# Performance work log

Measured on AMD Instinct MI355X. Metric: run time of the kernel, lower is better.

## Reference

```python
import jax, jax.numpy as jnp
import numpy as np

DIM = 512
HIDDEN = 512
HEADS = 8
HEAD_DIM = HIDDEN // HEADS
SCALE = HEAD_DIM ** -0.5
B, H, W = 2, 64, 64


def setup_inputs() -> dict:
    key = jax.random.key(0)
    ks = jax.random.split(key, 12)
    init = lambda k, shp: jax.random.normal(k, shp, dtype=jnp.float32) * 0.02
    return {
        "x": jax.random.normal(ks[0], (B, DIM, H, W), dtype=jnp.float32),
        "context": jax.random.normal(ks[1], (B, DIM, H, W), dtype=jnp.float32),
        # weights stored [in, out] so y = x @ W + b
        "Wi": init(ks[2], (DIM, HIDDEN)), "bi": jnp.zeros((HIDDEN,), jnp.float32),
        "Wc": init(ks[3], (DIM, HIDDEN)), "bc": jnp.zeros((HIDDEN,), jnp.float32),
        "Wq": init(ks[4], (HIDDEN, HIDDEN)),
        "Wk": init(ks[5], (HIDDEN, HIDDEN)),
        "Wv": init(ks[6], (HIDDEN, HIDDEN)),
        "Wo1": init(ks[7], (HIDDEN, HIDDEN)), "bo1": jnp.zeros((HIDDEN,), jnp.float32),
        "Wo2": init(ks[8], (HIDDEN, DIM)), "bo2": jnp.zeros((DIM,), jnp.float32),
    }


def reference(x, context, Wi, bi, Wc, bc, Wq, Wk, Wv, Wo1, bo1, Wo2, bo2):
    b, c, h, w = x.shape
    s = h * w
    x_seq = x.reshape(b, c, s).transpose(0, 2, 1)        # [B,S,C]
    ctx_seq = context.reshape(b, c, s).transpose(0, 2, 1)

    x_proj = x_seq @ Wi + bi                              # [B,S,Hid]
    ctx_proj = ctx_seq @ Wc + bc

    q = (x_proj @ Wq).reshape(b, s, HEADS, HEAD_DIM)      # [B,S,h,d]
    k = (ctx_proj @ Wk).reshape(b, s, HEADS, HEAD_DIM)
    v = (ctx_proj @ Wv).reshape(b, s, HEADS, HEAD_DIM)

    attn = jnp.einsum('bqhd,bkhd->bhqk', q, k) * SCALE    # [B,h,S,S]
    attn = jax.nn.softmax(attn, axis=-1)
    out = jnp.einsum('bhqk,bkhd->bqhd', attn, v).reshape(b, s, HIDDEN)

    out = jax.nn.gelu(out @ Wo1 + bo1, approximate=False) @ Wo2 + bo2  # [B,S,C]
    return out.transpose(0, 2, 1).reshape(b, c, h, w)
```

## Files before the change

### kernel.cpp

```cpp
#include <hip/hip_runtime.h>

#define SEQ 4096
#define CDIM 512
#define HID 512
#define NB 2
#define NHEADS 8

typedef float f32x4 __attribute__((ext_vector_type(4)));
typedef short bf16x8 __attribute__((ext_vector_type(8)));

static __device__ __forceinline__ short f2bf(float f) {
  unsigned u = __float_as_uint(f);
  u = (u + 0x7fffu + ((u >> 16) & 1u)) >> 16;
  return (short)u;
}
static __device__ __forceinline__ float bf2f(short h) {
  return __uint_as_float(((unsigned)(unsigned short)h) << 16);
}
static __device__ __forceinline__ unsigned pk2bf(float a, float b) {
  unsigned r;
  asm("v_cvt_pk_bf16_f32 %0, %1, %2" : "=v"(r) : "v"(a), "v"(b));
  return r;
}
typedef const __attribute__((address_space(1))) char gas_char;
typedef __attribute__((address_space(3))) char las_char;
static __device__ __forceinline__ void gll16(const char* g, char* l) {
  __builtin_amdgcn_global_load_lds((gas_char*)g, (las_char*)l, 16, 0, 0);
}

__global__ __launch_bounds__(256) void prep_w(
    const float* Wi, const float* Wc, const float* Wq, const float* Wk,
    const float* Wv, const float* Wo1, const float* Wo2,
    unsigned short* wth, unsigned short* wtl) {
  __shared__ float tile[32][33];
  const int z = blockIdx.z;
  const float* src;
  float scale = 1.0f;
  switch (z) {
    case 0: src = Wi; break;
    case 1: src = Wc; break;
    case 2: src = Wq; scale = 0.18033688011112042f; break;
    case 3: src = Wk; break;
    case 4: src = Wv; break;
    case 5: src = Wo1; break;
    default: src = Wo2; break;
  }
  const int n0 = blockIdx.x * 32, k0 = blockIdx.y * 32;
  const int tx = threadIdx.x, ty = threadIdx.y;
  for (int i = ty; i < 32; i += 8)
    tile[i][tx] = src[(k0 + i) * 512 + n0 + tx];
  __syncthreads();
  unsigned short* oh = wth + z * 262144;
  unsigned short* ol = wtl + z * 262144;
  for (int i = ty; i < 32; i += 8) {
    const float v = tile[tx][i] * scale;
    const short h = f2bf(v);
    oh[(n0 + i) * 512 + k0 + tx] = (unsigned short)h;
    ol[(n0 + i) * 512 + k0 + tx] = (unsigned short)f2bf(v - bf2f(h));
  }
}

__global__ __launch_bounds__(256) void prep_x2(
    const float* __restrict__ x, const float* __restrict__ ctx,
    unsigned short* __restrict__ oh0, unsigned short* __restrict__ ol0,
    unsigned short* __restrict__ oh1, unsigned short* __restrict__ ol1) {
  __shared__ float tile[32][33];
  const int b = blockIdx.z & 1;
  const int ten = blockIdx.z >> 1;
  const float* in = ten ? ctx : x;
  unsigned short* oh = ten ? oh1 : oh0;
  unsigned short* ol = ten ? ol1 : ol0;
  const int s0 = blockIdx.x * 32, c0 = blockIdx.y * 32;
  const int tx = threadIdx.x, ty = threadIdx.y;
  const float* ib = in + (long)b * CDIM * SEQ;
  for (int i = ty; i < 32; i += 8)
    tile[i][tx] = ib[(long)(c0 + i) * SEQ + s0 + tx];
  __syncthreads();
  const long ob = (long)b * SEQ * CDIM;
  for (int i = ty; i < 32; i += 8) {
    const float v = tile[tx][i];
    const short h = f2bf(v);
    oh[ob + (long)(s0 + i) * CDIM + c0 + tx] = (unsigned short)h;
    ol[ob + (long)(s0 + i) * CDIM + c0 + tx] = (unsigned short)f2bf(v - bf2f(h));
  }
}

#define OUT_DUAL 0
#define OUT_HI 1
#define OUT_F32 2

struct GemmJob {
  const unsigned short *Ah, *Al, *Wh, *Wl;
  const float* bias;
  void *outA, *outB;
  int tstore;
};

template <int OMODE, bool DO_GELU, bool HASB, int NJOBS>
__global__ __launch_bounds__(256) void gemmN(GemmJob J0, GemmJob J1, GemmJob J2) {
  __shared__ __align__(16) char lds[49152];
  const int orig = blockIdx.x + ((blockIdx.y + (blockIdx.z << 5)) << 3);
  const int work = (orig & 7) * (NJOBS * 64) + (orig >> 3);
  const int bx = work & 7;
  const int by = (work >> 3) & 31;
  const int bzz = work >> 8;
  const int jz = bzz >> 1;
  const int bz = bzz & 1;
  const GemmJob J = (NJOBS >= 3 && jz == 2) ? J2 : ((NJOBS >= 2 && jz == 1) ? J1 : J0);
  const int TS = J.tstore;
  const int t = threadIdx.x;
  const int lane = t & 63, wave = t >> 6;
  const int l15 = lane & 15, g = lane >> 4;
  const int m0 = by * 128, n0 = bx * 64;
  const long abase = (long)bz * SEQ * 512;

  const int grow = lane >> 3;
  const int ch = (((lane & 7) << 4) ^ (grow << 4));
  const int chp = ch & 63;
  const char* pa = (const char*)((ch < 64) ? J.Ah : J.Al);
  const char* pw = (const char*)((ch < 64) ? J.Wh : J.Wl);
  const char* aG[4];
#pragma unroll
  for (int i = 0; i < 4; ++i)
    aG[i] = pa + ((abase + (long)(m0 + wave * 32 + i * 8 + grow) * 512) << 1) + chp;
  const char* wG[2];
#pragma unroll
  for (int i = 0; i < 2; ++i)
    wG[i] = pw + (((long)(n0 + wave * 16 + i * 8 + grow) * 512) << 1) + chp;

  f32x4 acc[4][2];
#pragma unroll
  for (int p = 0; p < 4; ++p)
#pragma unroll
    for (int q = 0; q < 2; ++q) acc[p][q] = (f32x4){0.f, 0.f, 0.f, 0.f};

  {
    char* LA = lds;
    char* LW = lds + 16384;
#pragma unroll
    for (int i = 0; i < 4; ++i) gll16(aG[i], LA + wave * 4096 + i * 1024);
#pragma unroll
    for (int i = 0; i < 2; ++i) gll16(wG[i], LW + wave * 2048 + i * 1024);
  }

  int buf = 0;
  for (int k0 = 0; k0 < 512; k0 += 32) {
    char* LA = lds + buf * 24576;
    char* LW = LA + 16384;
    __syncthreads();
    if (k0 + 32 < 512) {
      char* NA = lds + (buf ^ 1) * 24576;
      char* NW = NA + 16384;
      const int koff = (k0 + 32) * 2;
#pragma unroll
      for (int i = 0; i < 4; ++i) gll16(aG[i] + koff, NA + wave * 4096 + i * 1024);
#pragma unroll
      for (int i = 0; i < 2; ++i) gll16(wG[i] + koff, NW + wave * 2048 + i * 1024);
    }

    if (!TS) {
      bf16x8 fbh[2], fbl[2];
#pragma unroll
      for (int q = 0; q < 2; ++q) {
        const int r = wave * 32 + q * 16 + l15;
        const char* rp = LA + r * 128;
        const int sw = (r & 7) << 4;
        fbh[q] = *(const bf16x8*)(rp + ((g << 4) ^ sw));
        fbl[q] = *(const bf16x8*)(rp + (((4 + g) << 4) ^ sw));
      }
#pragma unroll
      for (int p = 0; p < 4; ++p) {
        const int r = p * 16 + l15;
        const char* rp = LW + r * 128;
        const int sw = (r & 7) << 4;
        const bf16x8 fah = *(const bf16x8*)(rp + ((g << 4) ^ sw));
        const bf16x8 fal = *(const bf16x8*)(rp + (((4 + g) << 4) ^ sw));
#pragma unroll
        for (int q = 0; q < 2; ++q) {
          acc[p][q] = __builtin_amdgcn_mfma_f32_16x16x32_bf16(fah, fbh[q], acc[p][q], 0, 0, 0);
          acc[p][q] = __builtin_amdgcn_mfma_f32_16x16x32_bf16(fah, fbl[q], acc[p][q], 0, 0, 0);
          acc[p][q] = __builtin_amdgcn_mfma_f32_16x16x32_bf16(fal, fbh[q], acc[p][q], 0, 0, 0);
        }
      }
    } else {
      const int mB = (wave >> 1) * 64, nB = (wave & 1) * 32;
      bf16x8 fbh[2], fbl[2];
#pragma unroll
      for (int q = 0; q < 2; ++q) {
        const int r = nB + q * 16 + l15;
        const char* rp = LW + r * 128;
        const int sw = (r & 7) << 4;
        fbh[q] = *(const bf16x8*)(rp + ((g << 4) ^ sw));
        fbl[q] = *(const bf16x8*)(rp + (((4 + g) << 4) ^ sw));
      }
#pragma unroll
      for (int p = 0; p < 4; ++p) {
        const int r = mB + p * 16 + l15;
        const char* rp = LA + r * 128;
        const int sw = (r & 7) << 4;
        const bf16x8 fah = *(const bf16x8*)(rp + ((g << 4) ^ sw));
        const bf16x8 fal = *(const bf16x8*)(rp + (((4 + g) << 4) ^ sw));
#pragma unroll
        for (int q = 0; q < 2; ++q) {
          acc[p][q] = __builtin_amdgcn_mfma_f32_16x16x32_bf16(fah, fbh[q], acc[p][q], 0, 0, 0);
          acc[p][q] = __builtin_amdgcn_mfma_f32_16x16x32_bf16(fah, fbl[q], acc[p][q], 0, 0, 0);
          acc[p][q] = __builtin_amdgcn_mfma_f32_16x16x32_bf16(fal, fbh[q], acc[p][q], 0, 0, 0);
        }
      }
    }
    buf ^= 1;
  }

  const long obase = (long)bz * 512 * SEQ;
#pragma unroll
  for (int p = 0; p < 4; ++p)
#pragma unroll
    for (int q = 0; q < 2; ++q) {
      f32x4 v = acc[p][q];
      if (TS) {
        const int m = m0 + (wave >> 1) * 64 + p * 16 + 4 * g;
        const int n = n0 + (wave & 1) * 32 + q * 16 + l15;
        if (HASB) {
          const float b = J.bias[n];
          v[0] += b; v[1] += b; v[2] += b; v[3] += b;
        }
        if (OMODE == OUT_F32) {
          float4 f;
          f.x = v[0]; f.y = v[1]; f.z = v[2]; f.w = v[3];
          *(float4*)((float*)J.outA + obase + (long)n * SEQ + m) = f;
        } else {
          const short4 h4 = make_short4(f2bf(v[0]), f2bf(v[1]), f2bf(v[2]), f2bf(v[3]));
          *(short4*)((unsigned short*)J.outA + obase + (long)n * SEQ + m) = h4;
        }
      } else {
        const int n = n0 + p * 16 + 4 * g;
        const int m = m0 + wave * 32 + q * 16 + l15;
        if (HASB) v += *(const f32x4*)(J.bias + n);
        if (DO_GELU) {
#pragma unroll
          for (int r = 0; r < 4; ++r)
            v[r] = 0.5f * v[r] * (1.0f + erff(v[r] * 0.7071067811865476f));
        }
        unsigned short* oA = (unsigned short*)J.outA + obase + (long)m * 512 + n;
        if (OMODE == OUT_DUAL) {
          short h[4], l[4];
#pragma unroll
          for (int r = 0; r < 4; ++r) {
            h[r] = f2bf(v[r]);
            l[r] = f2bf(v[r] - bf2f(h[r]));
          }
          *(short4*)oA = make_short4(h[0], h[1], h[2], h[3]);
          *(short4*)((unsigned short*)J.outB + obase + (long)m * 512 + n) =
              make_short4(l[0], l[1], l[2], l[3]);
        } else {
          *(short4*)oA = make_short4(f2bf(v[0]), f2bf(v[1]), f2bf(v[2]), f2bf(v[3]));
        }
      }
    }
}

__global__ __launch_bounds__(512) void attn_mfma(
    const unsigned short* __restrict__ qh, const unsigned short* __restrict__ kh,
    const unsigned short* __restrict__ vt, unsigned short* __restrict__ oh,
    unsigned short* __restrict__ ol) {
  __shared__ __align__(16) char smem[32768];
  const int t = threadIdx.x;
  const int lane = t & 63;
  const int wave = t >> 6;
  const int l15 = lane & 15;
  const int g = lane >> 4;
  const int orig = blockIdx.x + ((blockIdx.y + (blockIdx.z << 3)) << 4);
  const int work = ((orig & 7) << 5) + (orig >> 3);
  const int hd = (work >> 4) & 7;
  const int bz = work >> 7;
  const int q0 = (work & 15) * 256;
  const long sbase = (long)bz * SEQ * 512;
  const long tbase = (long)bz * 512 * SEQ;

  const int grow = lane >> 3;
  const int ch = (((lane & 7) << 4) ^ (grow << 4));
  const char* kG = (const char*)kh + (sbase << 1) + hd * 128 +
                   (long)(wave * 8 + grow) * 1024 + ch;
  const char* vG = (const char*)vt +
                   ((tbase + (long)(hd * 64 + wave * 8 + grow) * 4096) << 1) + ch;

  const int swzl = (l15 & 7) << 4;
  const int kfb = l15 * 128 + g * 16;
  const int vfb = l15 * 128 + g * 8;

  bf16x8 qf[2][2];
#pragma unroll
  for (int u = 0; u < 2; ++u) {
    const unsigned short* qrow =
        qh + sbase + (long)(q0 + wave * 32 + u * 16 + l15) * 512 + hd * 64 + g * 8;
    qf[u][0] = *(const bf16x8*)(qrow);
    qf[u][1] = *(const bf16x8*)(qrow + 32);
  }

  bf16x8 vones;
#pragma unroll
  for (int e = 0; e < 8; ++e) vones[e] = (l15 == 0) ? (short)0x3f80 : (short)0;

  f32x4 acc[2][4];
  f32x4 acc5[2];
#pragma unroll
  for (int u = 0; u < 2; ++u) {
    acc5[u] = (f32x4){0.f, 0.f, 0.f, 0.f};
#pragma unroll
    for (int dt = 0; dt < 4; ++dt) acc[u][dt] = (f32x4){0.f, 0.f, 0.f, 0.f};
  }

  gll16(kG, smem + wave * 1024);
  gll16(vG, smem + 8192 + wave * 1024);

  int buf = 0;
  for (int j0 = 0; j0 < SEQ; j0 += 64) {
    char* Kl = smem + buf * 16384;
    char* Vl = Kl + 8192;
    __syncthreads();
    if (j0 + 64 < SEQ) {
      char* Kn = smem + (buf ^ 1) * 16384;
      gll16(kG + (long)(j0 + 64) * 1024, Kn + wave * 1024);
      gll16(vG + (long)(j0 + 64) * 2, Kn + 8192 + wave * 1024);
    }

    f32x4 st[2][4];
    __builtin_amdgcn_s_setprio(1);
#pragma unroll
    for (int kt = 0; kt < 4; ++kt) {
      const bf16x8 ka0 = *(const bf16x8*)(Kl + ((kt * 2048 + kfb) ^ swzl));
      const bf16x8 ka1 = *(const bf16x8*)(Kl + ((kt * 2048 + kfb + 64) ^ swzl));
      f32x4 s0 = {0.f, 0.f, 0.f, 0.f};
      f32x4 s1 = {0.f, 0.f, 0.f, 0.f};
      s0 = __builtin_amdgcn_mfma_f32_16x16x32_bf16(ka0, qf[0][0], s0, 0, 0, 0);
      s0 = __builtin_amdgcn_mfma_f32_16x16x32_bf16(ka1, qf[0][1], s0, 0, 0, 0);
      s1 = __builtin_amdgcn_mfma_f32_16x16x32_bf16(ka0, qf[1][0], s1, 0, 0, 0);
      s1 = __builtin_amdgcn_mfma_f32_16x16x32_bf16(ka1, qf[1][1], s1, 0, 0, 0);
      st[0][kt] = s0;
      st[1][kt] = s1;
    }
    __builtin_amdgcn_s_setprio(0);

    union Pb { bf16x8 v8; unsigned u4[4]; } pb[2][2];
#pragma unroll
    for (int u = 0; u < 2; ++u) {
#pragma unroll
      for (int kt = 0; kt < 4; ++kt)
#pragma unroll
        for (int r = 0; r < 4; ++r)
          st[u][kt][r] = __builtin_amdgcn_exp2f(st[u][kt][r]);
#pragma unroll
      for (int kc = 0; kc < 2; ++kc)
#pragma unroll
        for (int h = 0; h < 2; ++h) {
          pb[u][kc].u4[h * 2 + 0] = pk2bf(st[u][2 * kc + h][0], st[u][2 * kc + h][1]);
          pb[u][kc].u4[h * 2 + 1] = pk2bf(st[u][2 * kc + h][2], st[u][2 * kc + h][3]);
        }
    }

    __builtin_amdgcn_s_setprio(1);
#pragma unroll
    for (int dt = 0; dt < 4; ++dt) {
      union { bf16x8 v8; int2 h2[2]; } va0, va1;
      va0.h2[0] = *(const int2*)(Vl + ((dt * 2048 + vfb) ^ swzl));
      va0.h2[1] = *(const int2*)(Vl + ((dt * 2048 + vfb + 32) ^ swzl));
      va1.h2[0] = *(const int2*)(Vl + ((dt * 2048 + vfb + 64) ^ swzl));
      va1.h2[1] = *(const int2*)(Vl + ((dt * 2048 + vfb + 96) ^ swzl));
      acc[0][dt] = __builtin_amdgcn_mfma_f32_16x16x32_bf16(va0.v8, pb[0][0].v8, acc[0][dt], 0, 0, 0);
      acc[0][dt] = __builtin_amdgcn_mfma_f32_16x16x32_bf16(va1.v8, pb[0][1].v8, acc[0][dt], 0, 0, 0);
      acc[1][dt] = __builtin_amdgcn_mfma_f32_16x16x32_bf16(va0.v8, pb[1][0].v8, acc[1][dt], 0, 0, 0);
      acc[1][dt] = __builtin_amdgcn_mfma_f32_16x16x32_bf16(va1.v8, pb[1][1].v8, acc[1][dt], 0, 0, 0);
    }
#pragma unroll
    for (int u = 0; u < 2; ++u) {
      acc5[u] = __builtin_amdgcn_mfma_f32_16x16x32_bf16(vones, pb[u][0].v8, acc5[u], 0, 0, 0);
      acc5[u] = __builtin_amdgcn_mfma_f32_16x16x32_bf16(vones, pb[u][1].v8, acc5[u], 0, 0, 0);
    }
    __builtin_amdgcn_s_setprio(0);
    buf ^= 1;
  }

#pragma unroll
  for (int u = 0; u < 2; ++u) {
    const float lt = __shfl(acc5[u][0], l15);
    const float inv = 1.0f / lt;
    const long orow = sbase + (long)(q0 + wave * 32 + u * 16 + l15) * 512 + hd * 64;
#pragma unroll
    for (int dt = 0; dt < 4; ++dt) {
      short h[4], l[4];
#pragma unroll
      for (int r = 0; r < 4; ++r) {
        const float v = acc[u][dt][r] * inv;
        h[r] = f2bf(v);
        l[r] = f2bf(v - bf2f(h[r]));
      }
      *(short4*)(oh + orow + dt * 16 + g * 4) = make_short4(h[0], h[1], h[2], h[3]);
      *(short4*)(ol + orow + dt * 16 + g * 4) = make_short4(l[0], l[1], l[2], l[3]);
    }
  }
}

extern "C" void kernel_launch(void* const* d_in, const int* in_sizes, int n_in,
                              void* d_out, int out_size, void* d_ws,
                              size_t ws_size, hipStream_t stream) {
  const float* x   = (const float*)d_in[0];
  const float* ctx = (const float*)d_in[1];
  const float* Wi  = (const float*)d_in[2];
  const float* bi  = (const float*)d_in[3];
  const float* Wc  = (const float*)d_in[4];
  const float* bc  = (const float*)d_in[5];
  const float* Wq  = (const float*)d_in[6];
  const float* Wk  = (const float*)d_in[7];
  const float* Wv  = (const float*)d_in[8];
  const float* Wo1 = (const float*)d_in[9];
  const float* bo1 = (const float*)d_in[10];
  const float* Wo2 = (const float*)d_in[11];
  const float* bo2 = (const float*)d_in[12];
  float* out = (float*)d_out;

  char* p = (char*)d_ws;
  unsigned short* wth = (unsigned short*)p; p += (size_t)7 * 262144 * 2;
  unsigned short* wtl = (unsigned short*)p; p += (size_t)7 * 262144 * 2;
  const size_t PLE = (size_t)NB * SEQ * 512;
  unsigned short* P1 = (unsigned short*)p; p += PLE * 2;
  unsigned short* P2 = (unsigned short*)p; p += PLE * 2;
  unsigned short* P3 = (unsigned short*)p; p += PLE * 2;
  unsigned short* P4 = (unsigned short*)p; p += PLE * 2;
  unsigned short* P5 = (unsigned short*)p; p += PLE * 2;
  unsigned short* P6 = (unsigned short*)p; p += PLE * 2;
  unsigned short* P7 = (unsigned short*)d_out;
  unsigned short* P8 = P7 + PLE;

  const dim3 gb(256);
  const dim3 pg(16, 16, 7), pbk(32, 8);
  const dim3 xg(128, 16, 2 * NB);
  GemmJob jn = {};

  prep_w<<<pg, pbk, 0, stream>>>(Wi, Wc, Wq, Wk, Wv, Wo1, Wo2, wth, wtl);
  prep_x2<<<xg, pbk, 0, stream>>>(x, ctx, P1, P2, P3, P4);
  {
    GemmJob ja = {P1, P2, wth + 0 * 262144, wtl + 0 * 262144, bi, P5, P6, 0};
    GemmJob jb = {P3, P4, wth + 1 * 262144, wtl + 1 * 262144, bc, P7, P8, 0};
    gemmN<OUT_DUAL, false, true, 2><<<dim3(8, 32, 4), gb, 0, stream>>>(ja, jb, jn);
  }
  {
    GemmJob ja = {P5, P6, wth + 2 * 262144, wtl + 2 * 262144, nullptr, P1, nullptr, 0};
    GemmJob jb = {P7, P8, wth + 3 * 262144, wtl + 3 * 262144, nullptr, P2, nullptr, 0};
    GemmJob jc = {P7, P8, wth + 4 * 262144, wtl + 4 * 262144, nullptr, P3, nullptr, 1};
    gemmN<OUT_HI, false, false, 3><<<dim3(8, 32, 6), gb, 0, stream>>>(ja, jb, jc);
  }
  attn_mfma<<<dim3(SEQ / 256, NHEADS, NB), dim3(512), 0, stream>>>(P1, P2, P3, P4, P5);
  {
    GemmJob j = {P4, P5, wth + 5 * 262144, wtl + 5 * 262144, bo1, P6, P1, 0};
    gemmN<OUT_DUAL, true, true, 1><<<dim3(8, 32, 2), gb, 0, stream>>>(j, jn, jn);
  }
  {
    GemmJob j = {P6, P1, wth + 6 * 262144, wtl + 6 * 262144, bo2, out, nullptr, 1};
    gemmN<OUT_F32, false, true, 1><<<dim3(8, 32, 2), gb, 0, stream>>>(j, jn, jn);
  }
}
```

Measured before the change: 227.1 us.

## Fold input projections into Q/K/V weights to remove a sequence-length GEMM stage

Precomputes the combined weights Wi·Wq, Wc·Wk and Wc·Wv (and the matching folded biases) as small 512x512 GEMMs. The Q/K/V projections can then be applied directly to the split-bf16 inputs, skipping the first full-sequence GEMM and its hi/lo intermediate writes. It adds a tiny GEMM launch, a serial bias kernel, and extra rounding in the products of the folded weights. The GEMM kernel is generalised with grid-shape template parameters to handle the small weight-product grid.

```diff
diff --git a/kernel.cpp b/kernel.cpp
--- a/kernel.cpp
+++ b/kernel.cpp
@@ -52,12 +52,35 @@
   __syncthreads();
   unsigned short* oh = wth + z * 262144;
   unsigned short* ol = wtl + z * 262144;
-  for (int i = ty; i < 32; i += 8) {
-    const float v = tile[tx][i] * scale;
-    const short h = f2bf(v);
-    oh[(n0 + i) * 512 + k0 + tx] = (unsigned short)h;
-    ol[(n0 + i) * 512 + k0 + tx] = (unsigned short)f2bf(v - bf2f(h));
-  }
+  if (z < 2) {
+    for (int i = ty; i < 32; i += 8) {
+      const float v = tile[i][tx];
+      const short h = f2bf(v);
+      oh[(k0 + i) * 512 + n0 + tx] = (unsigned short)h;
+      ol[(k0 + i) * 512 + n0 + tx] = (unsigned short)f2bf(v - bf2f(h));
+    }
+  } else {
+    for (int i = ty; i < 32; i += 8) {
+      const float v = tile[tx][i] * scale;
+      const short h = f2bf(v);
+      oh[(n0 + i) * 512 + k0 + tx] = (unsigned short)h;
+      ol[(n0 + i) * 512 + k0 + tx] = (unsigned short)f2bf(v - bf2f(h));
+    }
+  }
+}
+
+__global__ __launch_bounds__(512) void prep_bias(
+    const float* __restrict__ bi, const float* __restrict__ Wq,
+    const float* __restrict__ bc, const float* __restrict__ Wk,
+    const float* __restrict__ Wv, float* __restrict__ bout) {
+  const int z = blockIdx.x;
+  const int n = threadIdx.x;
+  const float* b = (z == 0) ? bi : bc;
+  const float* W = (z == 0) ? Wq : (z == 1) ? Wk : Wv;
+  const float s = (z == 0) ? 0.18033688011112042f : 1.0f;
+  float acc = 0.0f;
+  for (int k = 0; k < 512; ++k) acc += b[k] * W[k * 512 + n];
+  bout[z * 512 + n] = acc * s;
 }
 
 __global__ __launch_bounds__(256) void prep_x2(
@@ -96,16 +119,18 @@
   int tstore;
 };
 
-template <int OMODE, bool DO_GELU, bool HASB, int NJOBS>
+template <int OMODE, bool DO_GELU, bool HASB, int NJOBS, int GY, int NBATCH>
 __global__ __launch_bounds__(256) void gemmN(GemmJob J0, GemmJob J1, GemmJob J2) {
   __shared__ __align__(16) char lds[49152];
-  const int orig = blockIdx.x + ((blockIdx.y + (blockIdx.z << 5)) << 3);
-  const int work = (orig & 7) * (NJOBS * 64) + (orig >> 3);
+  const int orig = blockIdx.x + ((blockIdx.y + blockIdx.z * GY) << 3);
+  const int total = 8 * GY * NBATCH * NJOBS;
+  const int work = (orig & 7) * (total >> 3) + (orig >> 3);
   const int bx = work & 7;
-  const int by = (work >> 3) & 31;
-  const int bzz = work >> 8;
-  const int jz = bzz >> 1;
-  const int bz = bzz & 1;
+  const int rest = work >> 3;
+  const int by = rest % GY;
+  const int z = rest / GY;
+  const int jz = z / NBATCH;
+  const int bz = z % NBATCH;
   const GemmJob J = (NJOBS >= 3 && jz == 2) ? J2 : ((NJOBS >= 2 && jz == 1) ? J1 : J0);
   const int TS = J.tstore;
   const int t = threadIdx.x;
@@ -418,9 +443,13 @@
   const float* bo2 = (const float*)d_in[12];
   float* out = (float*)d_out;
 
+  const size_t WP = 262144;
   char* p = (char*)d_ws;
-  unsigned short* wth = (unsigned short*)p; p += (size_t)7 * 262144 * 2;
-  unsigned short* wtl = (unsigned short*)p; p += (size_t)7 * 262144 * 2;
+  unsigned short* wth = (unsigned short*)p; p += (size_t)7 * WP * 2;
+  unsigned short* wtl = (unsigned short*)p; p += (size_t)7 * WP * 2;
+  unsigned short* cwh = (unsigned short*)p; p += (size_t)3 * WP * 2;
+  unsigned short* cwl = (unsigned short*)p; p += (size_t)3 * WP * 2;
+  float* bqkv = (float*)p; p += 3 * 512 * 4;
   const size_t PLE = (size_t)NB * SEQ * 512;
   unsigned short* P1 = (unsigned short*)p; p += PLE * 2;
   unsigned short* P2 = (unsigned short*)p; p += PLE * 2;
@@ -429,7 +458,6 @@
   unsigned short* P5 = (unsigned short*)p; p += PLE * 2;
   unsigned short* P6 = (unsigned short*)p; p += PLE * 2;
   unsigned short* P7 = (unsigned short*)d_out;
-  unsigned short* P8 = P7 + PLE;
 
   const dim3 gb(256);
   const dim3 pg(16, 16, 7), pbk(32, 8);
@@ -437,25 +465,30 @@
   GemmJob jn = {};
 
   prep_w<<<pg, pbk, 0, stream>>>(Wi, Wc, Wq, Wk, Wv, Wo1, Wo2, wth, wtl);
+  prep_bias<<<dim3(3), dim3(512), 0, stream>>>(bi, Wq, bc, Wk, Wv, bqkv);
   prep_x2<<<xg, pbk, 0, stream>>>(x, ctx, P1, P2, P3, P4);
   {
-    GemmJob ja = {P1, P2, wth + 0 * 262144, wtl + 0 * 262144, bi, P5, P6, 0};
-    GemmJob jb = {P3, P4, wth + 1 * 262144, wtl + 1 * 262144, bc, P7, P8, 0};
-    gemmN<OUT_DUAL, false, true, 2><<<dim3(8, 32, 4), gb, 0, stream>>>(ja, jb, jn);
+    GemmJob ja = {wth + 2 * WP, wtl + 2 * WP, wth + 0 * WP, wtl + 0 * WP,
+                  nullptr, cwh + 0 * WP, cwl + 0 * WP, 0};
+    GemmJob jb = {wth + 3 * WP, wtl + 3 * WP, wth + 1 * WP, wtl + 1 * WP,
+                  nullptr, cwh + 1 * WP, cwl + 1 * WP, 0};
+    GemmJob jc = {wth + 4 * WP, wtl + 4 * WP, wth + 1 * WP, wtl + 1 * WP,
+                  nullptr, cwh + 2 * WP, cwl + 2 * WP, 0};
+    gemmN<OUT_DUAL, false, false, 3, 4, 1><<<dim3(8, 4, 3), gb, 0, stream>>>(ja, jb, jc);
   }
   {
-    GemmJob ja = {P5, P6, wth + 2 * 262144, wtl + 2 * 262144, nullptr, P1, nullptr, 0};
-    GemmJob jb = {P7, P8, wth + 3 * 262144, wtl + 3 * 262144, nullptr, P2, nullptr, 0};
-    GemmJob jc = {P7, P8, wth + 4 * 262144, wtl + 4 * 262144, nullptr, P3, nullptr, 1};
-    gemmN<OUT_HI, false, false, 3><<<dim3(8, 32, 6), gb, 0, stream>>>(ja, jb, jc);
-  }
-  attn_mfma<<<dim3(SEQ / 256, NHEADS, NB), dim3(512), 0, stream>>>(P1, P2, P3, P4, P5);
+    GemmJob ja = {P1, P2, cwh + 0 * WP, cwl + 0 * WP, bqkv + 0, P5, nullptr, 0};
+    GemmJob jb = {P3, P4, cwh + 1 * WP, cwl + 1 * WP, bqkv + 512, P6, nullptr, 0};
+    GemmJob jc = {P3, P4, cwh + 2 * WP, cwl + 2 * WP, bqkv + 1024, P7, nullptr, 1};
+    gemmN<OUT_HI, false, true, 3, 32, 2><<<dim3(8, 32, 6), gb, 0, stream>>>(ja, jb, jc);
+  }
+  attn_mfma<<<dim3(SEQ / 256, NHEADS, NB), dim3(512), 0, stream>>>(P5, P6, P7, P1, P2);
   {
-    GemmJob j = {P4, P5, wth + 5 * 262144, wtl + 5 * 262144, bo1, P6, P1, 0};
-    gemmN<OUT_DUAL, true, true, 1><<<dim3(8, 32, 2), gb, 0, stream>>>(j, jn, jn);
+    GemmJob j = {P1, P2, wth + 5 * WP, wtl + 5 * WP, bo1, P3, P4, 0};
+    gemmN<OUT_DUAL, true, true, 1, 32, 2><<<dim3(8, 32, 2), gb, 0, stream>>>(j, jn, jn);
   }
   {
-    GemmJob j = {P6, P1, wth + 6 * 262144, wtl + 6 * 262144, bo2, out, nullptr, 1};
-    gemmN<OUT_F32, false, true, 1><<<dim3(8, 32, 2), gb, 0, stream>>>(j, jn, jn);
-  }
-}
+    GemmJob j = {P3, P4, wth + 6 * WP, wtl + 6 * WP, bo2, out, nullptr, 1};
+    gemmN<OUT_F32, false, true, 1, 32, 2><<<dim3(8, 32, 2), gb, 0, stream>>>(j, jn, jn);
+  }
+}
```

Measured after the change: 214.9 us (median of 2 runs). -5.4%, faster.
